# Performance work log

Measured on AMD Instinct MI355X. Metric: run time of the kernel, lower is better.

The kernel has to match this reference:

```python
import jax, jax.numpy as jnp
import numpy as np

H = 8  # num_heads
EPS = 1e-6


def _pos_encoding(S, D):
    # absolute sinusoidal positional encoding, shape [S, D]
    pos = jnp.arange(S, dtype=jnp.float32)[:, None]
    div = jnp.exp(jnp.arange(0, D, 2, dtype=jnp.float32) * (-np.log(10000.0) / D))
    pe = jnp.zeros((S, D), dtype=jnp.float32)
    pe = pe.at[:, 0::2].set(jnp.sin(pos * div))
    pe = pe.at[:, 1::2].set(jnp.cos(pos * div))
    return pe


def setup_inputs() -> dict:
    key = jax.random.key(0)
    ks = jax.random.split(key, 5)
    S, B, D = 2048, 16, 1024
    s = 1.0 / np.sqrt(D)
    return {
        'x': jax.random.normal(ks[0], (S, B, D), dtype=jnp.float32),
        'Wq': jax.random.normal(ks[1], (D, D), dtype=jnp.float32) * s,
        'bq': jnp.zeros((D,), dtype=jnp.float32),
        'Wk': jax.random.normal(ks[2], (D, D), dtype=jnp.float32) * s,
        'bk': jnp.zeros((D,), dtype=jnp.float32),
        'Wv': jax.random.normal(ks[3], (D, D), dtype=jnp.float32) * s,
        'bv': jnp.zeros((D,), dtype=jnp.float32),
        'Wo': jax.random.normal(ks[4], (D, D), dtype=jnp.float32) * s,
        'bo': jnp.zeros((D,), dtype=jnp.float32),
    }


def reference(x, Wq, bq, Wk, bk, Wv, bv, Wo, bo):
    # x: [S, B, D]  (nn.Transformer layout)
    S, B, D = x.shape
    dh = D // H
    h = x + _pos_encoding(S, D)[:, None, :]
    # projections (torch Linear: y = x @ W.T + b), split into heads
    q = (h @ Wq.T + bq).reshape(S, B, H, dh)
    k = (h @ Wk.T + bk).reshape(S, B, H, dh)
    v = (h @ Wv.T + bv).reshape(S, B, H, dh)
    # kernel feature map phi(u) = elu(u) + 1 (Katharopoulos linear attention)
    pq = jax.nn.elu(q) + 1.0
    pk = jax.nn.elu(k) + 1.0
    # global (non-causal) linear attention:
    # kv state: sum_s phi(k_s) v_s^T  -> [B, H, dh, dh]
    kv = jnp.einsum('sbhd,sbhe->bhde', pk, v)
    # normalizer: sum_s phi(k_s)     -> [B, H, dh]
    z = pk.sum(axis=0)
    num = jnp.einsum('sbhd,bhde->sbhe', pq, kv)   # [S, B, H, dh]
    den = jnp.einsum('sbhd,bhd->sbh', pq, z)       # [S, B, H]
    att = num / (den[..., None] + EPS)
    out = att.reshape(S, B, D) @ Wo.T + bo
    return out
```

## Files before the change

kernel.cpp:

```cpp
#include <hip/hip_runtime.h>
#include <hip/hip_bf16.h>
#include <stdint.h>


typedef __bf16 bf16x8 __attribute__((ext_vector_type(8)));
typedef float f32x4 __attribute__((ext_vector_type(4)));

#define S_LEN 2048
#define B_SZ  16
#define D_MOD 1024
#define N_H   8
#define D_H   128

__device__ __forceinline__ short f2bf(float f) {
  __bf16 b = (__bf16)f;
  return __builtin_bit_cast(short, b);
}
__device__ __forceinline__ float bf2f(short s) {
  return (float)__builtin_bit_cast(__bf16, s);
}

__device__ __forceinline__ void gload_lds16(const short* g, short* l) {
  __builtin_amdgcn_global_load_lds(
      (__attribute__((address_space(1))) void*)(g),
      (__attribute__((address_space(3))) void*)(l), 16, 0, 0);
}

__device__ __forceinline__ int swz(int o) { return o ^ (((o >> 7) & 3) << 4); }

__device__ __forceinline__ bf16x8 ld_bf8_8al(const short* p) {
  union { unsigned long long u[2]; bf16x8 v; } x;
  x.u[0] = *(const unsigned long long*)p;
  x.u[1] = *(const unsigned long long*)(p + 4);
  return x.v;
}

__global__ void prep_h(const float* __restrict__ x, short* __restrict__ h) {
  size_t idx8 = (size_t)blockIdx.x * blockDim.x + threadIdx.x;
  size_t base = idx8 * 8;
  int d = (int)(base & 1023);
  int r = (int)(base >> 10);
  int s = r >> 4;
  float4 v0 = *(const float4*)(x + base);
  float4 v1 = *(const float4*)(x + base + 4);
  float vs[8] = {v0.x, v0.y, v0.z, v0.w, v1.x, v1.y, v1.z, v1.w};
  const float kdiv = -9.210340371976184f / 1024.0f;
  bf16x8 ov;
#pragma unroll
  for (int t = 0; t < 8; ++t) {
    int dc = d + t;
    float div = __expf((float)(dc & ~1) * kdiv);
    float ang = (float)s * div;
    float pe = (dc & 1) ? __cosf(ang) : __sinf(ang);
    ov[t] = (__bf16)(vs[t] + pe);
  }
  *(bf16x8*)(h + base) = ov;
}

__global__ void pack_w(const float* __restrict__ Wq, const float* __restrict__ Wk,
                       const float* __restrict__ Wv, const float* __restrict__ Wo,
                       short* __restrict__ Wcat) {
  size_t i4 = (size_t)blockIdx.x * blockDim.x + threadIdx.x;
  size_t base = i4 * 4;
  const float* src;
  size_t off;
  if (base < 1048576)      { src = Wq; off = base; }
  else if (base < 2097152) { src = Wk; off = base - 1048576; }
  else if (base < 3145728) { src = Wv; off = base - 2097152; }
  else                     { src = Wo; off = base - 3145728; }
  float4 v = *(const float4*)(src + off);
  alignas(8) short o[4] = {f2bf(v.x), f2bf(v.y), f2bf(v.z), f2bf(v.w)};
  *(uint2*)(Wcat + base) = *(const uint2*)o;
}

template <int K>
__device__ __forceinline__ void core_256(const short* __restrict__ A,
                                         const short* __restrict__ W,
                                         char* Lb, f32x4 (&acc)[8][4]) {
  constexpr int NT = K / 32;
  static_assert(NT >= 4, "pipeline needs K >= 128");
  const int tid = threadIdx.x;
  const int lane = tid & 63;
  const int wave = tid >> 6;
  const int wm = wave & 1, wn = wave >> 1;
  const int l15 = lane & 15, quad = lane >> 4;

  const int oA0 = tid * 16, oA1 = 8192 + tid * 16;
  const int lA0 = swz(oA0), lA1 = swz(oA1);
  const short* gA0 = A + (size_t)(lA0 >> 6) * K + ((lA0 & 63) >> 1);
  const short* gA1 = A + (size_t)((lA1 - 8192) >> 6) * K + 128 * K + (((lA1 - 8192) & 63) >> 1);
  const short* gW0 = W + (size_t)(lA0 >> 6) * K + ((lA0 & 63) >> 1);
  const short* gW1 = W + (size_t)((lA1 - 8192) >> 6) * K + 128 * K + (((lA1 - 8192) & 63) >> 1);

  int rA[8], rW[4];
#pragma unroll
  for (int i = 0; i < 8; ++i)
    rA[i] = swz((wm * 128 + i * 16 + l15) * 64 + quad * 16);
#pragma unroll
  for (int j = 0; j < 4; ++j)
    rW[j] = 16384 + swz((wn * 64 + j * 16 + l15) * 64 + quad * 16);

  auto stage = [&](int t) {
    char* sb = Lb + (t & 3) * 32768;
    const int k0 = t * 32;
    gload_lds16(gA0 + k0, (short*)(sb + oA0));
    gload_lds16(gA1 + k0, (short*)(sb + oA1));
    gload_lds16(gW0 + k0, (short*)(sb + 16384 + oA0));
    gload_lds16(gW1 + k0, (short*)(sb + 16384 + oA1));
  };
  auto step = [&](int t, bool do_stage) {
    char* cb = Lb + (t & 3) * 32768;
    bf16x8 af[8], wf[4];
#pragma unroll
    for (int i = 0; i < 8; ++i) af[i] = *(const bf16x8*)(cb + rA[i]);
#pragma unroll
    for (int j = 0; j < 4; ++j) wf[j] = *(const bf16x8*)(cb + rW[j]);
    if (do_stage) stage(t + 3);
    __builtin_amdgcn_s_setprio(1);
#pragma unroll
    for (int i = 0; i < 8; ++i)
#pragma unroll
      for (int j = 0; j < 4; ++j)
        acc[i][j] = __builtin_amdgcn_mfma_f32_16x16x32_bf16(af[i], wf[j], acc[i][j], 0, 0, 0);
    __builtin_amdgcn_s_setprio(0);
    asm volatile("s_waitcnt lgkmcnt(0)" ::: "memory");
    __builtin_amdgcn_sched_barrier(0);
  };

  stage(0); stage(1); stage(2);

  for (int t = 0; t <= NT - 4; ++t) {
    asm volatile("s_waitcnt vmcnt(8)" ::: "memory");
    __builtin_amdgcn_s_barrier();
    step(t, true);
  }
  asm volatile("s_waitcnt vmcnt(8)" ::: "memory");
  __builtin_amdgcn_s_barrier();
  step(NT - 3, false);
  asm volatile("s_waitcnt vmcnt(4)" ::: "memory");
  __builtin_amdgcn_s_barrier();
  step(NT - 2, false);
  asm volatile("s_waitcnt vmcnt(0)" ::: "memory");
  __builtin_amdgcn_s_barrier();
  step(NT - 1, false);
}

template <int K>
__device__ __forceinline__ void core_128(const short* __restrict__ A,
                                         const short* __restrict__ W,
                                         char* Lb, f32x4 (&acc)[4][4]) {
  constexpr int NT = K / 32;
  static_assert(NT >= 4, "pipeline needs K >= 128");
  const int tid = threadIdx.x;
  const int lane = tid & 63;
  const int wm = (tid >> 6) & 1, wn = tid >> 7;
  const int l15 = lane & 15, quad = lane >> 4;

  const int oA0 = tid * 16, oA1 = 4096 + tid * 16;
  const int lA0 = swz(oA0), lA1 = swz(oA1);
  const short* gA0 = A + (size_t)(lA0 >> 6) * K + ((lA0 & 63) >> 1);
  const short* gA1 = A + (size_t)((lA1 - 4096) >> 6) * K + 64 * K + (((lA1 - 4096) & 63) >> 1);
  const short* gW0 = W + (size_t)(lA0 >> 6) * K + ((lA0 & 63) >> 1);
  const short* gW1 = W + (size_t)((lA1 - 4096) >> 6) * K + 64 * K + (((lA1 - 4096) & 63) >> 1);

  int rA[4], rW[4];
#pragma unroll
  for (int i = 0; i < 4; ++i)
    rA[i] = swz((wm * 64 + i * 16 + l15) * 64 + quad * 16);
#pragma unroll
  for (int j = 0; j < 4; ++j)
    rW[j] = 8192 + swz((wn * 64 + j * 16 + l15) * 64 + quad * 16);

  auto stage = [&](int t) {
    char* sb = Lb + (t & 3) * 16384;
    const int k0 = t * 32;
    gload_lds16(gA0 + k0, (short*)(sb + oA0));
    gload_lds16(gA1 + k0, (short*)(sb + oA1));
    gload_lds16(gW0 + k0, (short*)(sb + 8192 + oA0));
    gload_lds16(gW1 + k0, (short*)(sb + 8192 + oA1));
  };
  auto step = [&](int t, bool do_stage) {
    char* cb = Lb + (t & 3) * 16384;
    bf16x8 af[4], wf[4];
#pragma unroll
    for (int i = 0; i < 4; ++i) af[i] = *(const bf16x8*)(cb + rA[i]);
#pragma unroll
    for (int j = 0; j < 4; ++j) wf[j] = *(const bf16x8*)(cb + rW[j]);
    if (do_stage) stage(t + 3);
    __builtin_amdgcn_s_setprio(1);
#pragma unroll
    for (int i = 0; i < 4; ++i)
#pragma unroll
      for (int j = 0; j < 4; ++j)
        acc[i][j] = __builtin_amdgcn_mfma_f32_16x16x32_bf16(af[i], wf[j], acc[i][j], 0, 0, 0);
    __builtin_amdgcn_s_setprio(0);
    asm volatile("s_waitcnt lgkmcnt(0)" ::: "memory");
    __builtin_amdgcn_sched_barrier(0);
  };

  stage(0); stage(1); stage(2);

  for (int t = 0; t <= NT - 4; ++t) {
    asm volatile("s_waitcnt vmcnt(8)" ::: "memory");
    __builtin_amdgcn_s_barrier();
    step(t, true);
  }
  asm volatile("s_waitcnt vmcnt(8)" ::: "memory");
  __builtin_amdgcn_s_barrier();
  step(NT - 3, false);
  asm volatile("s_waitcnt vmcnt(4)" ::: "memory");
  __builtin_amdgcn_s_barrier();
  step(NT - 2, false);
  asm volatile("s_waitcnt vmcnt(0)" ::: "memory");
  __builtin_amdgcn_s_barrier();
  step(NT - 1, false);
}

__launch_bounds__(512, 2)
__global__ void gemm_qkv(const short* __restrict__ h, const short* __restrict__ Wqkv,
                         const float* __restrict__ bq, const float* __restrict__ bk,
                         const float* __restrict__ bv,
                         short* __restrict__ pq, short* __restrict__ pk,
                         short* __restrict__ pv) {
  __shared__ alignas(16) char Lb[131072];
  const int lin = blockIdx.y * 12 + blockIdx.x;
  const int x = lin & 7, q = lin >> 3;
  const int xm = x >> 1, xn = x & 1;
  const int bm = xm * 32 + q / 6;
  const int bn = xn * 6 + q % 6;
  const int rowBase = bm * 256, colBase = bn * 256;

  f32x4 acc[8][4] = {};
  core_256<1024>(h + (size_t)rowBase * 1024, Wqkv + (size_t)colBase * 1024, Lb, acc);

  const int tid = threadIdx.x;
  const int lane = tid & 63;
  const int wave = tid >> 6;
  const int wm = wave & 1, wn = wave >> 1;
  const int l15 = lane & 15, quad = lane >> 4;

  const int p = bn >> 2;
  const float* bias = (p == 0) ? bq : (p == 1) ? bk : bv;
  short* Pout = (p == 0) ? pq : (p == 1) ? pk : pv;

  __syncthreads();
  short* Lt = (short*)Lb;
#pragma unroll
  for (int j = 0; j < 4; ++j) {
    const int c = wn * 64 + j * 16 + l15;
    const float bval = bias[(bn & 3) * 256 + c];
#pragma unroll
    for (int i = 0; i < 8; ++i) {
#pragma unroll
      for (int r = 0; r < 4; ++r) {
        const int mloc = wm * 128 + i * 16 + quad * 4 + r;
        float v = acc[i][j][r] + bval;
        if (p < 2) v = v > 0.f ? v + 1.f : __expf(v);
        Lt[mloc * 256 + (c ^ ((mloc & 7) << 3))] = f2bf(v);
      }
    }
  }
  __syncthreads();
  const int g16 = tid >> 4, L = tid & 15;
#pragma unroll
  for (int it = 0; it < 16; ++it) {
    const int chunk = it * 32 + g16;
    const int row = chunk >> 1, hhl = chunk & 1;
    const int grow = rowBase + row;
    const int s = grow >> 4, b = grow & 15;
    const int hh = (bn & 3) * 2 + hhl;
    const short* src = Lt + row * 256 + ((hhl * 128 + L * 8) ^ ((row & 7) << 3));
    short* dst = Pout + (((size_t)b * N_H + hh) * S_LEN + s) * D_H + L * 8;
    *(uint4*)dst = *(const uint4*)src;
  }
}

__launch_bounds__(256, 2)
__global__ void kv_kernel(const short* __restrict__ pk, const short* __restrict__ pv,
                          short* __restrict__ kvT, float* __restrict__ z) {
  __shared__ alignas(16) short Vt[128 * 44];
  __shared__ alignas(16) short Pt[128 * 44];
  __shared__ float zl[16 * 128];
  const int bh = blockIdx.x;
  const short* Vg = pv + (size_t)bh * S_LEN * D_H;
  const short* Pg = pk + (size_t)bh * S_LEN * D_H;

  const int tid = threadIdx.x;
  const int lane = tid & 63;
  const int wm = (tid >> 6) & 1, wn = tid >> 7;
  const int l15 = lane & 15, quad = lane >> 4;
  const int s_loc = tid >> 3, e8 = tid & 7;

  const short* vsrc = Vg + s_loc * 128 + e8 * 8;
  const short* psrc = Pg + s_loc * 128 + e8 * 8;

  f32x4 acc[4][4] = {};
  uint4 cv0, cv1, cp0, cp1;
  cv0 = *(const uint4*)(vsrc);
  cv1 = *(const uint4*)(vsrc + 64);
  cp0 = *(const uint4*)(psrc);
  cp1 = *(const uint4*)(psrc + 64);

  for (int t = 0; t < 64; ++t) {
    __builtin_amdgcn_s_barrier();
    const short* sv0 = (const short*)&cv0;
    const short* sv1 = (const short*)&cv1;
    const short* sp0 = (const short*)&cp0;
    const short* sp1 = (const short*)&cp1;
#pragma unroll
    for (int u = 0; u < 8; ++u) {
      Vt[(e8 * 8 + u) * 44 + s_loc] = sv0[u];
      Vt[(64 + e8 * 8 + u) * 44 + s_loc] = sv1[u];
      Pt[(e8 * 8 + u) * 44 + s_loc] = sp0[u];
      Pt[(64 + e8 * 8 + u) * 44 + s_loc] = sp1[u];
    }
    if (t < 63) {
      const int o = (t + 1) * 32 * 128;
      cv0 = *(const uint4*)(vsrc + o);
      cv1 = *(const uint4*)(vsrc + o + 64);
      cp0 = *(const uint4*)(psrc + o);
      cp1 = *(const uint4*)(psrc + o + 64);
    }
    asm volatile("s_waitcnt lgkmcnt(0)" ::: "memory");
    __builtin_amdgcn_sched_barrier(0);
    __builtin_amdgcn_s_barrier();
    bf16x8 af[4], wf[4];
#pragma unroll
    for (int i = 0; i < 4; ++i)
      af[i] = ld_bf8_8al(&Vt[(wm * 64 + i * 16 + l15) * 44 + quad * 8]);
#pragma unroll
    for (int j = 0; j < 4; ++j)
      wf[j] = ld_bf8_8al(&Pt[(wn * 64 + j * 16 + l15) * 44 + quad * 8]);
#pragma unroll
    for (int i = 0; i < 4; ++i)
#pragma unroll
      for (int j = 0; j < 4; ++j)
        acc[i][j] = __builtin_amdgcn_mfma_f32_16x16x32_bf16(af[i], wf[j], acc[i][j], 0, 0, 0);
    asm volatile("s_waitcnt lgkmcnt(0)" ::: "memory");
    __builtin_amdgcn_sched_barrier(0);
  }

#pragma unroll
  for (int j = 0; j < 4; ++j) {
    const int d = wn * 64 + j * 16 + l15;
#pragma unroll
    for (int i = 0; i < 4; ++i) {
#pragma unroll
      for (int r = 0; r < 4; ++r) {
        const int e = wm * 64 + i * 16 + quad * 4 + r;
        kvT[(size_t)bh * (D_H * D_H) + (size_t)e * D_H + d] = f2bf(acc[i][j][r]);
      }
    }
  }
  __syncthreads();
  {
    const int d8 = tid & 15, so = tid >> 4;
    float za[8] = {};
    for (int s = so; s < S_LEN; s += 16) {
      uint4 u = *(const uint4*)(Pg + (size_t)s * 128 + d8 * 8);
      const short* sp = (const short*)&u;
#pragma unroll
      for (int u2 = 0; u2 < 8; ++u2) za[u2] += bf2f(sp[u2]);
    }
#pragma unroll
    for (int u2 = 0; u2 < 8; ++u2) zl[so * 128 + d8 * 8 + u2] = za[u2];
  }
  __syncthreads();
  if (tid < 128) {
    float sum = 0.f;
#pragma unroll
    for (int k = 0; k < 16; ++k) sum += zl[k * 128 + tid];
    z[bh * D_H + tid] = sum;
  }
}

__launch_bounds__(256, 2)
__global__ void attn_kernel(const short* __restrict__ pq, const short* __restrict__ kvT,
                            const float* __restrict__ z, short* __restrict__ att) {
  __shared__ alignas(16) char Lb[65536];
  __shared__ float den_lds[128];
  __shared__ float z_lds[128];
  const int s0 = blockIdx.x * 128;
  const int bh = blockIdx.y;
  const int tid = threadIdx.x;

  const short* Abase = pq + ((size_t)bh * S_LEN + s0) * D_H;
  const short* Wbase = kvT + (size_t)bh * (D_H * D_H);

  f32x4 acc[4][4] = {};
  core_128<128>(Abase, Wbase, Lb, acc);

  if (tid < 128) z_lds[tid] = z[bh * D_H + tid];
  __syncthreads();
  if (tid < 128) {
    const short* prow = Abase + (size_t)tid * D_H;
    float sum = 0.f;
#pragma unroll
    for (int d = 0; d < D_H; d += 8) {
      bf16x8 vv = *(const bf16x8*)(prow + d);
#pragma unroll
      for (int t = 0; t < 8; ++t) sum += (float)vv[t] * z_lds[d + t];
    }
    den_lds[tid] = sum + 1e-6f;
  }
  __syncthreads();

  const int lane = tid & 63;
  const int wm = (tid >> 6) & 1, wn = tid >> 7;
  const int l15 = lane & 15, quad = lane >> 4;
  const int b = bh >> 3, hd = bh & 7;
#pragma unroll
  for (int j = 0; j < 4; ++j) {
    const int e = wn * 64 + j * 16 + l15;
#pragma unroll
    for (int i = 0; i < 4; ++i) {
#pragma unroll
      for (int r = 0; r < 4; ++r) {
        int mloc = wm * 64 + i * 16 + quad * 4 + r;
        float a = acc[i][j][r] / den_lds[mloc];
        att[((size_t)(s0 + mloc) * B_SZ + b) * D_MOD + hd * D_H + e] = f2bf(a);
      }
    }
  }
}

__launch_bounds__(512, 2)
__global__ void gemm_out(const short* __restrict__ att, const short* __restrict__ WoB,
                         const float* __restrict__ bo, float* __restrict__ out) {
  __shared__ alignas(16) char Lb[131072];
  const int lin = blockIdx.y * 4 + blockIdx.x;
  const int x = lin & 7, q = lin >> 3;
  const int bn = q & 3;
  const int bm = x * 16 + (q >> 2);
  const int rowBase = bm * 256, colBase = bn * 256;

  f32x4 acc[8][4] = {};
  core_256<1024>(att + (size_t)rowBase * 1024, WoB + (size_t)colBase * 1024, Lb, acc);

  const int tid = threadIdx.x;
  const int lane = tid & 63;
  const int wave = tid >> 6;
  const int wm = wave & 1, wn = wave >> 1;
  const int l15 = lane & 15, quad = lane >> 4;
#pragma unroll
  for (int j = 0; j < 4; ++j) {
    const int gcol = colBase + wn * 64 + j * 16 + l15;
    const float bval = bo[gcol];
#pragma unroll
    for (int i = 0; i < 8; ++i) {
#pragma unroll
      for (int r = 0; r < 4; ++r) {
        int grow = rowBase + wm * 128 + i * 16 + quad * 4 + r;
        out[(size_t)grow * 1024 + gcol] = acc[i][j][r] + bval;
      }
    }
  }
}

extern "C" void kernel_launch(void* const* d_in, const int* in_sizes, int n_in,
                              void* d_out, int out_size, void* d_ws, size_t ws_size,
                              hipStream_t stream) {
  const float* x  = (const float*)d_in[0];
  const float* Wq = (const float*)d_in[1];
  const float* bq = (const float*)d_in[2];
  const float* Wk = (const float*)d_in[3];
  const float* bk = (const float*)d_in[4];
  const float* Wv = (const float*)d_in[5];
  const float* bv = (const float*)d_in[6];
  const float* Wo = (const float*)d_in[7];
  const float* bo = (const float*)d_in[8];
  float* out = (float*)d_out;

  char* ws = (char*)d_ws;
  short* h    = (short*)(ws);
  short* Wcat = (short*)(ws + 67108864);
  short* pq   = (short*)(ws + 75497472);
  short* pk   = (short*)(ws + 142606336);
  short* pv   = (short*)(ws + 209715200);
  short* kvT  = (short*)(ws + 276824064);
  float* z    = (float*)(ws + 281018368);

  prep_h<<<16384, 256, 0, stream>>>(x, h);
  pack_w<<<4096, 256, 0, stream>>>(Wq, Wk, Wv, Wo, Wcat);
  gemm_qkv<<<dim3(12, 128), 512, 0, stream>>>(h, Wcat, bq, bk, bv, pq, pk, pv);
  kv_kernel<<<128, 256, 0, stream>>>(pk, pv, kvT, z);
  attn_kernel<<<dim3(16, 128), 256, 0, stream>>>(pq, kvT, z, h );
  gemm_out<<<dim3(4, 128), 512, 0, stream>>>(h, Wcat + 3145728, bo, out);
}
```

Baseline: 685.6 us.

## Split kv state reduction over sequence chunks and compute denominator from LDS

The kv/z accumulation kernel now splits the sequence into 4 chunks per (batch, head), giving 512 blocks instead of 128 so more CUs are busy. A new reduction kernel sums the fp32 partials and converts them to bf16. The attention kernel also computes the denominator from the swizzled pq tile already staged in LDS instead of rereading global memory. The cost is an extra launch and an fp32 partial buffer written over the idle h workspace.

```diff
diff --git a/kernel.cpp b/kernel.cpp
--- a/kernel.cpp
+++ b/kernel.cpp
@@ -276,14 +276,16 @@
 }
 
 __launch_bounds__(256, 2)
-__global__ void kv_kernel(const short* __restrict__ pk, const short* __restrict__ pv,
-                          short* __restrict__ kvT, float* __restrict__ z) {
+__global__ void kv_part(const short* __restrict__ pk, const short* __restrict__ pv,
+                        float* __restrict__ kvp, float* __restrict__ zp) {
   __shared__ alignas(16) short Vt[128 * 44];
   __shared__ alignas(16) short Pt[128 * 44];
   __shared__ float zl[16 * 128];
-  const int bh = blockIdx.x;
-  const short* Vg = pv + (size_t)bh * S_LEN * D_H;
-  const short* Pg = pk + (size_t)bh * S_LEN * D_H;
+  const int split = blockIdx.x;
+  const int bh = blockIdx.y;
+  const int sbase = split * 512;
+  const short* Vg = pv + ((size_t)bh * S_LEN + sbase) * D_H;
+  const short* Pg = pk + ((size_t)bh * S_LEN + sbase) * D_H;
 
   const int tid = threadIdx.x;
   const int lane = tid & 63;
@@ -301,7 +303,7 @@
   cp0 = *(const uint4*)(psrc);
   cp1 = *(const uint4*)(psrc + 64);
 
-  for (int t = 0; t < 64; ++t) {
+  for (int t = 0; t < 16; ++t) {
     __builtin_amdgcn_s_barrier();
     const short* sv0 = (const short*)&cv0;
     const short* sv1 = (const short*)&cv1;
@@ -314,7 +316,7 @@
       Pt[(e8 * 8 + u) * 44 + s_loc] = sp0[u];
       Pt[(64 + e8 * 8 + u) * 44 + s_loc] = sp1[u];
     }
-    if (t < 63) {
+    if (t < 15) {
       const int o = (t + 1) * 32 * 128;
       cv0 = *(const uint4*)(vsrc + o);
       cv1 = *(const uint4*)(vsrc + o + 64);
@@ -340,6 +342,7 @@
     __builtin_amdgcn_sched_barrier(0);
   }
 
+  float* kout = kvp + (size_t)(bh * 4 + split) * (D_H * D_H);
 #pragma unroll
   for (int j = 0; j < 4; ++j) {
     const int d = wn * 64 + j * 16 + l15;
@@ -348,7 +351,7 @@
 #pragma unroll
       for (int r = 0; r < 4; ++r) {
         const int e = wm * 64 + i * 16 + quad * 4 + r;
-        kvT[(size_t)bh * (D_H * D_H) + (size_t)e * D_H + d] = f2bf(acc[i][j][r]);
+        kout[(size_t)e * D_H + d] = acc[i][j][r];
       }
     }
   }
@@ -356,7 +359,7 @@
   {
     const int d8 = tid & 15, so = tid >> 4;
     float za[8] = {};
-    for (int s = so; s < S_LEN; s += 16) {
+    for (int s = so; s < 512; s += 16) {
       uint4 u = *(const uint4*)(Pg + (size_t)s * 128 + d8 * 8);
       const short* sp = (const short*)&u;
 #pragma unroll
@@ -370,7 +373,22 @@
     float sum = 0.f;
 #pragma unroll
     for (int k = 0; k < 16; ++k) sum += zl[k * 128 + tid];
-    z[bh * D_H + tid] = sum;
+    zp[(bh * 4 + split) * D_H + tid] = sum;
+  }
+}
+
+__global__ void kv_reduce(const float* __restrict__ kvp, const float* __restrict__ zp,
+                          short* __restrict__ kvT, float* __restrict__ z) {
+  const int bh = blockIdx.x;
+  const int tid = threadIdx.x;
+  const float* k0 = kvp + (size_t)(bh * 4) * (D_H * D_H);
+  for (int i = tid; i < D_H * D_H; i += 256) {
+    float s = k0[i] + k0[16384 + i] + k0[32768 + i] + k0[49152 + i];
+    kvT[(size_t)bh * (D_H * D_H) + i] = f2bf(s);
+  }
+  if (tid < 128) {
+    const float* z0 = zp + bh * 4 * D_H;
+    z[bh * D_H + tid] = z0[tid] + z0[D_H + tid] + z0[2 * D_H + tid] + z0[3 * D_H + tid];
   }
 }
 
@@ -393,13 +411,20 @@
   if (tid < 128) z_lds[tid] = z[bh * D_H + tid];
   __syncthreads();
   if (tid < 128) {
-    const short* prow = Abase + (size_t)tid * D_H;
     float sum = 0.f;
 #pragma unroll
-    for (int d = 0; d < D_H; d += 8) {
-      bf16x8 vv = *(const bf16x8*)(prow + d);
-#pragma unroll
-      for (int t = 0; t < 8; ++t) sum += (float)vv[t] * z_lds[d + t];
+    for (int t = 0; t < 4; ++t) {
+      const char* Ab = Lb + t * 16384;
+#pragma unroll
+      for (int c8 = 0; c8 < 2; ++c8) {
+        bf16x8 vv = *(const bf16x8*)(Ab + swz(tid * 64 + c8 * 32));
+        bf16x8 vw = *(const bf16x8*)(Ab + swz(tid * 64 + c8 * 32 + 16));
+#pragma unroll
+        for (int u = 0; u < 8; ++u) {
+          sum += (float)vv[u] * z_lds[t * 32 + c8 * 16 + u];
+          sum += (float)vw[u] * z_lds[t * 32 + c8 * 16 + 8 + u];
+        }
+      }
     }
     den_lds[tid] = sum + 1e-6f;
   }
@@ -479,11 +504,14 @@
   short* pv   = (short*)(ws + 209715200);
   short* kvT  = (short*)(ws + 276824064);
   float* z    = (float*)(ws + 281018368);
+  float* kvp  = (float*)(ws);
+  float* zp   = (float*)(ws + 33554432);
 
   prep_h<<<16384, 256, 0, stream>>>(x, h);
   pack_w<<<4096, 256, 0, stream>>>(Wq, Wk, Wv, Wo, Wcat);
   gemm_qkv<<<dim3(12, 128), 512, 0, stream>>>(h, Wcat, bq, bk, bv, pq, pk, pv);
-  kv_kernel<<<128, 256, 0, stream>>>(pk, pv, kvT, z);
+  kv_part<<<dim3(4, 128), 256, 0, stream>>>(pk, pv, kvp, zp);
+  kv_reduce<<<128, 256, 0, stream>>>(kvp, zp, kvT, z);
   attn_kernel<<<dim3(16, 128), 256, 0, stream>>>(pq, kvT, z, h );
   gemm_out<<<dim3(4, 128), 512, 0, stream>>>(h, Wcat + 3145728, bo, out);
 }
```

Measured after the change: 651.9 us. 1.05x faster.
